# Kernel optimization log

Measured on AMD Instinct MI355X. Metric: run time of the kernel, lower is better.

## Reference

```python
import jax, jax.numpy as jnp
import numpy as np

B, N, E, D, H, C, U = 512, 256, 1024, 256, 256, 8, 64
MARGIN_T, RISK_T, SCALE = 0.2, 0.6, 0.1
NEG = -1.0e9


def setup_inputs() -> dict:
    key = jax.random.key(0)
    ks = jax.random.split(key, 30)
    s = 0.02
    inp = dict(
        features=jax.random.normal(ks[0], (B, D), jnp.float32),
        centered_scores=jax.random.normal(ks[1], (B, N), jnp.float32),
        margin=jax.random.uniform(ks[2], (B,), jnp.float32),
        boundary_risk=jax.random.uniform(ks[3], (B,), jnp.float32),
        edge_sensitivity=jax.random.normal(ks[4], (B, E), jnp.float32),
        coords=jax.random.normal(ks[5], (B, N, C), jnp.float32),
        uncertainty=jax.random.uniform(ks[6], (B, U), jnp.float32),
        Wc1=jax.random.normal(ks[7], (D, H), jnp.float32) * s,
        bc1=jnp.zeros((H,), jnp.float32),
        Wc2=jax.random.normal(ks[8], (H, H), jnp.float32) * s,
        bc2=jnp.zeros((H,), jnp.float32),
        Wn1=jax.random.normal(ks[9], (H + C + 2, H), jnp.float32) * s,
        bn1=jnp.zeros((H,), jnp.float32),
        Wn2=jax.random.normal(ks[10], (H, 1), jnp.float32) * s,
        bn2=jnp.zeros((1,), jnp.float32),
        We1=jax.random.normal(ks[11], (H + C + 2, H), jnp.float32) * s,
        be1=jnp.zeros((H,), jnp.float32),
        We2=jax.random.normal(ks[12], (H, 1), jnp.float32) * s,
        be2=jnp.zeros((1,), jnp.float32),
        Wg=jax.random.normal(ks[13], (H, 1), jnp.float32) * s,
        bg=jnp.zeros((1,), jnp.float32),
        action_mask=jax.random.bernoulli(ks[14], 0.8, (B, N)),
        edge_mask=jax.random.bernoulli(ks[15], 0.8, (B, E)),
        actions=jax.random.randint(ks[16], (B, N), 0, U, jnp.int32),
        edges=jax.random.randint(ks[17], (B, E, 2), 0, N, jnp.int32),
    )
    return inp


def _mlp2(x, W1, b1, W2, b2):
    return jax.nn.relu(x @ W1 + b1) @ W2 + b2


def reference(features, centered_scores, margin, boundary_risk, edge_sensitivity,
              coords, uncertainty, Wc1, bc1, Wc2, bc2, Wn1, bn1, Wn2, bn2,
              We1, be1, We2, be2, Wg, bg, action_mask, edge_mask, actions, edges):
    amf = action_mask.astype(jnp.float32)
    emf = edge_mask.astype(jnp.float32)

    # context MLP
    h = jax.nn.relu(jax.nn.relu(features @ Wc1 + bc1) @ Wc2 + bc2)  # [B,H]

    low_margin = (margin < MARGIN_T).astype(jnp.float32)
    high_risk = (boundary_risk > RISK_T).astype(jnp.float32)
    learned_gate = jax.nn.sigmoid((h @ Wg + bg)[:, 0])
    refine_gate = jnp.maximum(jnp.maximum(low_margin, high_risk),
                              (learned_gate > 0.5).astype(jnp.float32))  # [B]

    # node features: [B,N,H+C+2]
    act = jnp.clip(actions, 0, U - 1)
    unc_g = jnp.take_along_axis(uncertainty, act, axis=1)  # [B,N]
    h_n = jnp.broadcast_to(h[:, None, :], (B, N, H))
    node_feats = jnp.concatenate(
        [h_n, coords, centered_scores[..., None], unc_g[..., None]], axis=-1)
    node_delta = _mlp2(node_feats, Wn1, bn1, Wn2, bn2)[..., 0] * amf  # [B,N]

    # edge features: gather src/dst coords
    e = jnp.clip(edges, 0, N - 1)
    src_c = jnp.take_along_axis(coords, e[:, :, 0:1], axis=1)  # [B,E,C]
    dst_c = jnp.take_along_axis(coords, e[:, :, 1:2], axis=1)  # [B,E,C]
    h_e = jnp.broadcast_to(h[:, None, :], (B, E, H))
    edge_feats = jnp.concatenate(
        [h_e, dst_c - src_c, edge_sensitivity[..., None], emf[..., None]], axis=-1)
    edge_delta = _mlp2(edge_feats, We1, be1, We2, be2)[..., 0] * emf  # [B,E]

    gate_node = refine_gate[:, None]
    refined_scores = (centered_scores + gate_node * SCALE * node_delta) * amf
    denom = jnp.clip(amf.sum(-1, keepdims=True), 1.0, None)  # [B,1]
    refined_scores = (refined_scores - refined_scores.sum(-1, keepdims=True) / denom) * amf

    refined_edge = (edge_sensitivity + gate_node * SCALE * edge_delta) * emf

    masked_top = jnp.where(action_mask, refined_scores, NEG)
    top_vals, top_idx = jax.lax.top_k(masked_top, 2)
    refined_margin = top_vals[:, 0] - top_vals[:, 1]

    # masked per-batch variance of refined_edge (biased), 0 if <=1 valid entry
    cnt = emf.sum(-1)
    cnt_c = jnp.clip(cnt, 1.0, None)
    mean = (refined_edge * emf).sum(-1) / cnt_c
    var = (emf * (refined_edge - mean[:, None]) ** 2).sum(-1) / cnt_c
    edge_var = jnp.where(cnt > 1.0, var, 0.0)

    unc_term = (unc_g * amf).sum(-1) / denom[:, 0]
    refined_risk = jnp.clip(
        jax.nn.sigmoid(-refined_margin) + 0.2 * edge_var + 0.1 * unc_term, 0.0, 1.0)

    return (refined_scores, refined_margin, refined_edge,
            top_idx[:, 0], refined_risk, refine_gate)
```

## Files before the change

### kernel.cpp

```cpp
#include <hip/hip_runtime.h>
#include <math.h>

#define B 512
#define N 256
#define E 1024
#define D 256
#define H 256
#define C 8
#define U 64

typedef __fp16 h2 __attribute__((ext_vector_type(2)));
union UF { float f; h2 h; unsigned u; };

__device__ __forceinline__ float bc_f(h2 h) { UF u; u.h = h; return u.f; }
__device__ __forceinline__ h2 bc_h(float f) { UF u; u.f = f; return u.h; }

#if __has_builtin(__builtin_amdgcn_cvt_pkrtz)
__device__ __forceinline__ h2 pkh(float a, float b) { return __builtin_amdgcn_cvt_pkrtz(a, b); }
#else
__device__ __forceinline__ h2 pkh(float a, float b) { h2 r; r.x = (__fp16)a; r.y = (__fp16)b; return r; }
#endif

#if __has_builtin(__builtin_amdgcn_fdot2)
__device__ __forceinline__ float FDOT2(h2 a, h2 b, float c) { return __builtin_amdgcn_fdot2(a, b, c, false); }
#else
__device__ __forceinline__ float FDOT2(h2 a, h2 b, float c) {
    return fmaf((float)a.x, (float)b.x, fmaf((float)a.y, (float)b.y, c));
}
#endif

__device__ __forceinline__ float mask_val(const void* m, long i, int flag) {
    if (flag == 1) return ((const unsigned char*)m)[i] ? 1.f : 0.f;
    if (flag == 2) return (((const float*)m)[i] != 0.f) ? 1.f : 0.f;
    return ((const int*)m)[i] ? 1.f : 0.f;
}

__device__ __forceinline__ float block_sum(float v, float* red) {
    int t = threadIdx.x;
    red[t] = v; __syncthreads();
    for (int s = 128; s > 0; s >>= 1) {
        if (t < s) red[t] += red[t + s];
        __syncthreads();
    }
    float r = red[0]; __syncthreads();
    return r;
}

__global__ __launch_bounds__(512) void k_h(
    const float* __restrict__ feat,
    const float* __restrict__ Wc1, const float* __restrict__ bc1,
    const float* __restrict__ Wc2, const float* __restrict__ bc2,
    const float* __restrict__ Wn1, const float* __restrict__ bn1,
    const float* __restrict__ We1, const float* __restrict__ be1,
    const float* __restrict__ Wg,  const float* __restrict__ bg,
    const float* __restrict__ margin, const float* __restrict__ brisk,
    const unsigned int* __restrict__ amask_words,
    float* __restrict__ base_n, float* __restrict__ base_e,
    float* __restrict__ out_gate, int* __restrict__ flag,
    float* __restrict__ node_delta, float* __restrict__ out2)
{
    __shared__ __align__(16) float sF[4][256];
    __shared__ __align__(16) float sH[4][256];
    __shared__ float red[512];
    __shared__ int cls0, cls1;

    int t = threadIdx.x;
    int w = t >> 8;
    int c = t & 255;
    int b0 = blockIdx.x * 4;
    int r0 = 2 * w, r1 = 2 * w + 1;

    {
        int idx = blockIdx.x * 512 + t;
        node_delta[idx] = 0.f;
        node_delta[idx + 65536] = 0.f;
        float4 z4 = make_float4(0.f, 0.f, 0.f, 0.f);
        ((float4*)out2)[idx] = z4;
        ((float4*)out2)[idx + 65536] = z4;
    }

    if (blockIdx.x == 0) {
        if (t == 0) { cls0 = 0; cls1 = 0; }
        __syncthreads();
        if (t < 256) {
            unsigned int wd = amask_words[t];
            if (wd != 0u && wd != 1u) {
                if (wd == 0x3f800000u) atomicOr(&cls1, 1);
                else                   atomicOr(&cls0, 1);
            }
        }
        __syncthreads();
        if (t == 0) *flag = cls0 ? 1 : (cls1 ? 2 : 0);
    }

    sF[r0][c] = feat[(long)(b0 + r0) * D + c];
    sF[r1][c] = feat[(long)(b0 + r1) * D + c];
    __syncthreads();

    {
        float aA[2] = {bc1[c], 0.f}, aB[2] = {bc1[c], 0.f};
        const float* Wp = Wc1 + c;
        for (int d0 = 0; d0 < D; d0 += 16) {
            float wv[16];
            #pragma unroll
            for (int k = 0; k < 16; k++) wv[k] = Wp[(long)(d0 + k) * H];
            #pragma unroll
            for (int k = 0; k < 16; k++) {
                aA[k & 1] = fmaf(sF[r0][d0 + k], wv[k], aA[k & 1]);
                aB[k & 1] = fmaf(sF[r1][d0 + k], wv[k], aB[k & 1]);
            }
        }
        sH[r0][c] = fmaxf(aA[0] + aA[1], 0.f);
        sH[r1][c] = fmaxf(aB[0] + aB[1], 0.f);
    }
    __syncthreads();

    {
        float aA[2] = {bc2[c], 0.f}, aB[2] = {bc2[c], 0.f};
        const float* Wp = Wc2 + c;
        for (int d0 = 0; d0 < H; d0 += 16) {
            float wv[16];
            #pragma unroll
            for (int k = 0; k < 16; k++) wv[k] = Wp[(long)(d0 + k) * H];
            #pragma unroll
            for (int k = 0; k < 16; k++) {
                aA[k & 1] = fmaf(sH[r0][d0 + k], wv[k], aA[k & 1]);
                aB[k & 1] = fmaf(sH[r1][d0 + k], wv[k], aB[k & 1]);
            }
        }
        float hA = fmaxf(aA[0] + aA[1], 0.f);
        float hB = fmaxf(aB[0] + aB[1], 0.f);
        __syncthreads();
        sF[r0][c] = hA;
        sF[r1][c] = hB;
    }
    __syncthreads();

    #pragma unroll
    for (int rr = 0; rr < 2; rr++) {
        int r = 2 * w + rr;
        red[t] = sF[r][c] * Wg[c];
        __syncthreads();
        for (int s = 128; s > 0; s >>= 1) {
            if (c < s) red[t] += red[t + s];
            __syncthreads();
        }
        if (c == 0) {
            int b = b0 + r;
            float lg = 1.f / (1.f + expf(-(red[t] + bg[0])));
            out_gate[b] = ((margin[b] < 0.2f) || (brisk[b] > 0.6f) || (lg > 0.5f)) ? 1.f : 0.f;
        }
        __syncthreads();
    }

    {
        const float* W3  = w ? (We1 + c) : (Wn1 + c);
        float bias       = w ? be1[c]    : bn1[c];
        float* dst       = w ? base_e    : base_n;
        float aA[2] = {bias, 0.f}, aB[2] = {bias, 0.f};
        float aC[2] = {bias, 0.f}, aD[2] = {bias, 0.f};
        for (int d0 = 0; d0 < H; d0 += 16) {
            float wv[16];
            #pragma unroll
            for (int k = 0; k < 16; k++) wv[k] = W3[(long)(d0 + k) * H];
            #pragma unroll
            for (int k = 0; k < 16; k++) {
                aA[k & 1] = fmaf(sF[0][d0 + k], wv[k], aA[k & 1]);
                aB[k & 1] = fmaf(sF[1][d0 + k], wv[k], aB[k & 1]);
                aC[k & 1] = fmaf(sF[2][d0 + k], wv[k], aC[k & 1]);
                aD[k & 1] = fmaf(sF[3][d0 + k], wv[k], aD[k & 1]);
            }
        }
        dst[(long)(b0 + 0) * H + c] = aA[0] + aA[1];
        dst[(long)(b0 + 1) * H + c] = aB[0] + aB[1];
        dst[(long)(b0 + 2) * H + c] = aC[0] + aC[1];
        dst[(long)(b0 + 3) * H + c] = aD[0] + aD[1];
    }
}

__global__ __launch_bounds__(256, 2) void k_ne(
    const float* __restrict__ cs, const float* __restrict__ coords,
    const float* __restrict__ unc, const int* __restrict__ actions,
    const float* __restrict__ Wn1, const float* __restrict__ Wn2,
    const float* __restrict__ base_n,
    const float* __restrict__ es, const int* __restrict__ edges,
    const float* __restrict__ We1, const float* __restrict__ We2,
    const float* __restrict__ base_e,
    const float* __restrict__ gate,
    float* __restrict__ node_delta, float* __restrict__ out2)
{
    __shared__ __align__(16) float smem[4096];
    int t = threadIdx.x;
    int w = t >> 6, lane = t & 63;

    if (blockIdx.x < 256) {
        int rg = blockIdx.x >> 1;
        int jh = blockIdx.x & 1;
        int b0 = rg * 4;
        float* pack = smem;
        float* sB   = smem + 1536;

        if (t < 128) {
            float* p = pack + t * 12;
            int j = jh * 128 + t;
            #pragma unroll
            for (int k = 0; k < 10; k++) p[k] = Wn1[(long)(H + k) * H + j];
            p[10] = Wn2[j];
            p[11] = 0.f;
        }
        {
            int r = t >> 7, c0 = t & 127;
            sB[r * 128 + c0]       = base_n[(long)(b0 + r) * H + jh * 128 + c0];
            sB[(r + 2) * 128 + c0] = base_n[(long)(b0 + r + 2) * H + jh * 128 + c0];
        }
        __syncthreads();

        int b = b0 + w;
        float g = gate[b];
        if (g != 0.f) {
            float f8v[4], ug[4], acc[4];
            float f0[4], f1[4], f2[4], f3[4], f4[4], f5[4], f6[4], f7[4];
            #pragma unroll
            for (int q = 0; q < 4; q++) {
                int n = q * 64 + lane;
                const float4* cp = (const float4*)(coords + ((long)b * N + n) * C);
                float4 c0 = cp[0], c1 = cp[1];
                f0[q] = c0.x; f1[q] = c0.y; f2[q] = c0.z; f3[q] = c0.w;
                f4[q] = c1.x; f5[q] = c1.y; f6[q] = c1.z; f7[q] = c1.w;
                f8v[q] = cs[(long)b * N + n];
                int a = actions[(long)b * N + n];
                a = min(max(a, 0), U - 1);
                ug[q] = unc[(long)b * U + a];
                acc[q] = 0.f;
            }

            const float* sBw = sB + w * 128;
            #pragma unroll 4
            for (int j = 0; j < 128; j++) {
                const float* pj = pack + j * 12;
                float4 wa = *(const float4*)(pj);
                float4 wb = *(const float4*)(pj + 4);
                float4 wc = *(const float4*)(pj + 8);
                float bse = sBw[j];
                #pragma unroll
                for (int q = 0; q < 4; q++) {
                    float zA = fmaf(f0[q], wa.x, bse);
                    zA = fmaf(f1[q], wa.y, zA);
                    zA = fmaf(f2[q], wa.z, zA);
                    zA = fmaf(f3[q], wa.w, zA);
                    float zB = f4[q] * wb.x;
                    zB = fmaf(f5[q], wb.y, zB);
                    zB = fmaf(f6[q], wb.z, zB);
                    zB = fmaf(f7[q], wb.w, zB);
                    zB = fmaf(f8v[q], wc.x, zB);
                    zB = fmaf(ug[q], wc.y, zB);
                    acc[q] = fmaf(fmaxf(zA + zB, 0.f), wc.z, acc[q]);
                }
            }

            #pragma unroll
            for (int q = 0; q < 4; q++)
                atomicAdd(&node_delta[(long)b * N + q * 64 + lane], acc[q]);
        }
    } else {
        int eb = blockIdx.x - 256;
        int b = eb >> 1, jh = eb & 1;
        float g = gate[b];
        if (g == 0.f) return;

        float*  A4 = smem;
        float2* B2 = (float2*)(smem + 512);
        float*  sC = smem + 1024;

        {
            const float4* g4 = (const float4*)(coords + (long)b * N * C);
            float4 c0 = g4[2 * t], c1 = g4[2 * t + 1];
            float4* d0 = (float4*)(sC + t * 12);
            d0[0] = c0; d0[1] = c1;
        }
        if (t < 128) {
            int j = jh * 128 + t;
            float w0 = We1[(long)(H + 0) * H + j];
            float w1 = We1[(long)(H + 1) * H + j];
            float w2 = We1[(long)(H + 2) * H + j];
            float w3 = We1[(long)(H + 3) * H + j];
            float w4 = We1[(long)(H + 4) * H + j];
            float w5 = We1[(long)(H + 5) * H + j];
            float w6 = We1[(long)(H + 6) * H + j];
            float w7 = We1[(long)(H + 7) * H + j];
            float w8 = We1[(long)(H + 8) * H + j];
            float w9 = We1[(long)(H + 9) * H + j];
            float we2 = We2[j];
            float bse = base_e[(long)b * H + j] + w9;
            float4 av;
            av.x = bc_f(pkh(w0, w1)); av.y = bc_f(pkh(w2, w3));
            av.z = bc_f(pkh(w4, w5)); av.w = bc_f(pkh(w6, w7));
            ((float4*)A4)[t] = av;
            B2[t] = make_float2(bc_f(pkh(w8, we2)), bse);
        }
        __syncthreads();

        float p01[4], p23[4], p45[4], p67[4], pes[4], acc[4];
        #pragma unroll
        for (int q = 0; q < 4; q++) {
            int e = w * 256 + q * 64 + lane;
            long idx = (long)b * E + e;
            int2 ev = ((const int2*)edges)[idx];
            int s0 = min(max(ev.x, 0), N - 1);
            int d0 = min(max(ev.y, 0), N - 1);
            const float4* cs4 = (const float4*)(sC + s0 * 12);
            const float4* cd4 = (const float4*)(sC + d0 * 12);
            float4 sa = cs4[0], sb = cs4[1];
            float4 da = cd4[0], db = cd4[1];
            p01[q] = bc_f(pkh(da.x - sa.x, da.y - sa.y));
            p23[q] = bc_f(pkh(da.z - sa.z, da.w - sa.w));
            p45[q] = bc_f(pkh(db.x - sb.x, db.y - sb.y));
            p67[q] = bc_f(pkh(db.z - sb.z, db.w - sb.w));
            pes[q] = bc_f(pkh(es[idx], 0.f));
            acc[q] = 0.f;
        }

        const float4* A4v = (const float4*)A4;
        #pragma unroll 4
        for (int j = 0; j < 128; j++) {
            float4 av = A4v[j];
            float2 bv = B2[j];
            h2 w01 = bc_h(av.x), w23 = bc_h(av.y);
            h2 w45 = bc_h(av.z), w67 = bc_h(av.w);
            h2 w8x = bc_h(bv.x);
            float we2f = (float)(w8x.y);
            float bse = bv.y;
            #pragma unroll
            for (int q = 0; q < 4; q++) {
                float z = FDOT2(bc_h(p01[q]), w01, bse);
                z = FDOT2(bc_h(p23[q]), w23, z);
                z = FDOT2(bc_h(p45[q]), w45, z);
                z = FDOT2(bc_h(p67[q]), w67, z);
                z = FDOT2(bc_h(pes[q]), w8x, z);
                acc[q] = fmaf(fmaxf(z, 0.f), we2f, acc[q]);
            }
        }

        #pragma unroll
        for (int q = 0; q < 4; q++)
            atomicAdd(&out2[(long)b * E + w * 256 + q * 64 + lane], acc[q]);
    }
}

__global__ __launch_bounds__(256) void k_fin(
    const void* __restrict__ amask, const void* __restrict__ emask,
    const int* __restrict__ actions, const float* __restrict__ unc,
    const float* __restrict__ cs, const float* __restrict__ es,
    const float* __restrict__ bn2, const float* __restrict__ be2,
    const float* __restrict__ gate, const int* __restrict__ flagp,
    const float* __restrict__ node_delta,
    float* __restrict__ out0, float* __restrict__ out1,
    float* __restrict__ out2, float* __restrict__ out3,
    float* __restrict__ riskbase, float* __restrict__ evar)
{
    __shared__ float red[256];
    __shared__ int ridx[256];
    int t = threadIdx.x;
    int flag = *flagp;

    if (blockIdx.x < B) {
        int b = blockIdx.x;
        float g = gate[b];
        float am = mask_val(amask, (long)b * N + t, flag);
        float csv = cs[(long)b * N + t];
        int a = actions[(long)b * N + t];
        a = min(max(a, 0), U - 1);
        float ug = unc[(long)b * U + a];
        float nd = (node_delta[(long)b * N + t] + bn2[0]) * am;
        float raw = (csv + g * 0.1f * nd) * am;

        float sum = block_sum(raw, red);
        float cnt = block_sum(am, red);
        float denom = fmaxf(cnt, 1.f);
        float rs = (raw - sum / denom) * am;
        out0[(long)b * N + t] = rs;

        float masked = (am != 0.f) ? rs : -1e9f;

        red[t] = masked; ridx[t] = t; __syncthreads();
        for (int s = 128; s > 0; s >>= 1) {
            if (t < s) {
                float o = red[t + s]; int oi = ridx[t + s];
                if (o > red[t] || (o == red[t] && oi < ridx[t])) { red[t] = o; ridx[t] = oi; }
            }
            __syncthreads();
        }
        float v1 = red[0]; int i1 = ridx[0]; __syncthreads();

        red[t] = (t == i1) ? -1e9f : masked; __syncthreads();
        for (int s = 128; s > 0; s >>= 1) {
            if (t < s) red[t] = fmaxf(red[t], red[t + s]);
            __syncthreads();
        }
        float v2 = red[0]; __syncthreads();
        float rmargin = v1 - v2;

        float su = block_sum(ug * am, red);

        if (t == 0) {
            out1[b] = rmargin;
            out3[b] = (float)i1;
            float sig = 1.f / (1.f + expf(rmargin));
            riskbase[b] = sig + 0.1f * (su / denom);
        }
    } else {
        int b = blockIdx.x - B;
        float g = gate[b];
        float be2v = be2[0];

        float re[4], emv[4];
        #pragma unroll
        for (int q = 0; q < 4; q++) {
            long idx = (long)b * E + t + 256 * q;
            emv[q] = mask_val(emask, idx, flag);
            float delta = out2[idx] + be2v;
            float r = es[idx] + g * 0.1f * delta;
            re[q] = (emv[q] != 0.f) ? r : 0.f;
            out2[idx] = re[q];
        }

        float S1 = 0.f, ce = 0.f;
        #pragma unroll
        for (int q = 0; q < 4; q++) { S1 += re[q]; ce += emv[q]; }
        float S1t = block_sum(S1, red);
        float cet = block_sum(ce, red);
        float mean = S1t / fmaxf(cet, 1.f);
        float v = 0.f;
        #pragma unroll
        for (int q = 0; q < 4; q++) {
            float dd = re[q] - mean;
            v = fmaf(emv[q] * dd, dd, v);
        }
        float vt = block_sum(v, red);
        if (t == 0) {
            float var = vt / fmaxf(cet, 1.f);
            evar[b] = (cet > 1.f) ? var : 0.f;
        }
    }
}

__global__ __launch_bounds__(256) void k_risk(
    const float* __restrict__ riskbase, const float* __restrict__ evar,
    float* __restrict__ out4)
{
    int b = blockIdx.x * 256 + threadIdx.x;
    float r = riskbase[b] + 0.2f * evar[b];
    out4[b] = fminf(fmaxf(r, 0.f), 1.f);
}

extern "C" void kernel_launch(void* const* d_in, const int* in_sizes, int n_in,
                              void* d_out, int out_size, void* d_ws, size_t ws_size,
                              hipStream_t stream) {
    const float* feat   = (const float*)d_in[0];
    const float* cs     = (const float*)d_in[1];
    const float* marg   = (const float*)d_in[2];
    const float* brisk  = (const float*)d_in[3];
    const float* es     = (const float*)d_in[4];
    const float* coords = (const float*)d_in[5];
    const float* unc    = (const float*)d_in[6];
    const float* Wc1    = (const float*)d_in[7];
    const float* bc1    = (const float*)d_in[8];
    const float* Wc2    = (const float*)d_in[9];
    const float* bc2    = (const float*)d_in[10];
    const float* Wn1    = (const float*)d_in[11];
    const float* bn1    = (const float*)d_in[12];
    const float* Wn2    = (const float*)d_in[13];
    const float* bn2    = (const float*)d_in[14];
    const float* We1    = (const float*)d_in[15];
    const float* be1    = (const float*)d_in[16];
    const float* We2    = (const float*)d_in[17];
    const float* be2    = (const float*)d_in[18];
    const float* Wg     = (const float*)d_in[19];
    const float* bg     = (const float*)d_in[20];
    const void*  amask  = d_in[21];
    const void*  emask  = d_in[22];
    const int*   actions= (const int*)d_in[23];
    const int*   edges  = (const int*)d_in[24];

    float* out0 = (float*)d_out;
    float* out1 = out0 + (long)B * N;
    float* out2 = out1 + B;
    float* out3 = out2 + (long)B * E;
    float* out4 = out3 + B;
    float* out5 = out4 + B;

    float* base_n     = (float*)d_ws;
    float* base_e     = base_n + (long)B * H;
    float* node_delta = base_e + (long)B * H;
    float* riskbase   = node_delta + (long)B * N;
    float* evar       = riskbase + B;
    int*   flag       = (int*)(evar + B);

    k_h<<<B / 4, 512, 0, stream>>>(feat, Wc1, bc1, Wc2, bc2, Wn1, bn1, We1, be1,
                                   Wg, bg, marg, brisk,
                                   (const unsigned int*)amask,
                                   base_n, base_e, out5, flag,
                                   node_delta, out2);
    k_ne<<<256 + 2 * B, 256, 0, stream>>>(cs, coords, unc, actions,
                                          Wn1, Wn2, base_n,
                                          es, edges,
                                          We1, We2, base_e,
                                          out5, node_delta, out2);
    k_fin<<<2 * B, 256, 0, stream>>>(amask, emask, actions, unc, cs, es,
                                     bn2, be2, out5, flag, node_delta,
                                     out0, out1, out2, out3, riskbase, evar);
    k_risk<<<2, 256, 0, stream>>>(riskbase, evar, out4);
}
```

Baseline: 77.54 us.

## Double grid parallelism in context and node/edge kernels by splitting batch and hidden dims

The context-MLP kernel now handles 2 batch rows per block instead of 4, doubling its grid. Each thread accumulates one row with four partial sums instead of two rows with two. The node/edge kernel splits the hidden dimension into quarters instead of halves, doubling its block count and halving per-block work and shared memory. This gives more parallelism across the many CUs, at the cost of more redundant weight reads, more atomic adds into node_delta, and repeated per-block setup such as loading coordinates.

```diff
diff --git a/kernel.cpp b/kernel.cpp
--- a/kernel.cpp
+++ b/kernel.cpp
@@ -59,24 +59,21 @@
     float* __restrict__ out_gate, int* __restrict__ flag,
     float* __restrict__ node_delta, float* __restrict__ out2)
 {
-    __shared__ __align__(16) float sF[4][256];
-    __shared__ __align__(16) float sH[4][256];
+    __shared__ __align__(16) float sF[2][256];
+    __shared__ __align__(16) float sH[2][256];
     __shared__ float red[512];
     __shared__ int cls0, cls1;
 
     int t = threadIdx.x;
     int w = t >> 8;
     int c = t & 255;
-    int b0 = blockIdx.x * 4;
-    int r0 = 2 * w, r1 = 2 * w + 1;
+    int b0 = blockIdx.x * 2;
+    int b = b0 + w;
 
     {
         int idx = blockIdx.x * 512 + t;
         node_delta[idx] = 0.f;
-        node_delta[idx + 65536] = 0.f;
-        float4 z4 = make_float4(0.f, 0.f, 0.f, 0.f);
-        ((float4*)out2)[idx] = z4;
-        ((float4*)out2)[idx + 65536] = z4;
+        ((float4*)out2)[idx] = make_float4(0.f, 0.f, 0.f, 0.f);
     }
 
     if (blockIdx.x == 0) {
@@ -93,72 +90,58 @@
         if (t == 0) *flag = cls0 ? 1 : (cls1 ? 2 : 0);
     }
 
-    sF[r0][c] = feat[(long)(b0 + r0) * D + c];
-    sF[r1][c] = feat[(long)(b0 + r1) * D + c];
+    sF[w][c] = feat[(long)b * D + c];
     __syncthreads();
 
     {
-        float aA[2] = {bc1[c], 0.f}, aB[2] = {bc1[c], 0.f};
+        float acc[4] = {bc1[c], 0.f, 0.f, 0.f};
         const float* Wp = Wc1 + c;
         for (int d0 = 0; d0 < D; d0 += 16) {
             float wv[16];
             #pragma unroll
             for (int k = 0; k < 16; k++) wv[k] = Wp[(long)(d0 + k) * H];
             #pragma unroll
-            for (int k = 0; k < 16; k++) {
-                aA[k & 1] = fmaf(sF[r0][d0 + k], wv[k], aA[k & 1]);
-                aB[k & 1] = fmaf(sF[r1][d0 + k], wv[k], aB[k & 1]);
-            }
-        }
-        sH[r0][c] = fmaxf(aA[0] + aA[1], 0.f);
-        sH[r1][c] = fmaxf(aB[0] + aB[1], 0.f);
+            for (int k = 0; k < 16; k++)
+                acc[k & 3] = fmaf(sF[w][d0 + k], wv[k], acc[k & 3]);
+        }
+        sH[w][c] = fmaxf((acc[0] + acc[1]) + (acc[2] + acc[3]), 0.f);
     }
     __syncthreads();
 
     {
-        float aA[2] = {bc2[c], 0.f}, aB[2] = {bc2[c], 0.f};
+        float acc[4] = {bc2[c], 0.f, 0.f, 0.f};
         const float* Wp = Wc2 + c;
         for (int d0 = 0; d0 < H; d0 += 16) {
             float wv[16];
             #pragma unroll
             for (int k = 0; k < 16; k++) wv[k] = Wp[(long)(d0 + k) * H];
             #pragma unroll
-            for (int k = 0; k < 16; k++) {
-                aA[k & 1] = fmaf(sH[r0][d0 + k], wv[k], aA[k & 1]);
-                aB[k & 1] = fmaf(sH[r1][d0 + k], wv[k], aB[k & 1]);
-            }
-        }
-        float hA = fmaxf(aA[0] + aA[1], 0.f);
-        float hB = fmaxf(aB[0] + aB[1], 0.f);
-        __syncthreads();
-        sF[r0][c] = hA;
-        sF[r1][c] = hB;
+            for (int k = 0; k < 16; k++)
+                acc[k & 3] = fmaf(sH[w][d0 + k], wv[k], acc[k & 3]);
+        }
+        float a = fmaxf((acc[0] + acc[1]) + (acc[2] + acc[3]), 0.f);
+        __syncthreads();
+        sF[w][c] = a;
     }
     __syncthreads();
 
-    #pragma unroll
-    for (int rr = 0; rr < 2; rr++) {
-        int r = 2 * w + rr;
-        red[t] = sF[r][c] * Wg[c];
-        __syncthreads();
-        for (int s = 128; s > 0; s >>= 1) {
-            if (c < s) red[t] += red[t + s];
-            __syncthreads();
-        }
-        if (c == 0) {
-            int b = b0 + r;
-            float lg = 1.f / (1.f + expf(-(red[t] + bg[0])));
-            out_gate[b] = ((margin[b] < 0.2f) || (brisk[b] > 0.6f) || (lg > 0.5f)) ? 1.f : 0.f;
-        }
-        __syncthreads();
+    red[t] = sF[w][c] * Wg[c];
+    __syncthreads();
+    for (int s = 128; s > 0; s >>= 1) {
+        if (c < s) red[t] += red[t + s];
+        __syncthreads();
+    }
+    if (c == 0) {
+        float lg = 1.f / (1.f + expf(-(red[t] + bg[0])));
+        out_gate[b] = ((margin[b] < 0.2f) || (brisk[b] > 0.6f) || (lg > 0.5f)) ? 1.f : 0.f;
     }
 
     {
         const float* W3  = w ? (We1 + c) : (Wn1 + c);
         float bias       = w ? be1[c]    : bn1[c];
         float* dst       = w ? base_e    : base_n;
-        float aA[2] = {bias, 0.f}, aB[2] = {bias, 0.f};
-        float aC[2] = {bias, 0.f}, aD[2] = {bias, 0.f};
+        float aA[2] = {bias, 0.f};
+        float aB[2] = {bias, 0.f};
         for (int d0 = 0; d0 < H; d0 += 16) {
             float wv[16];
             #pragma unroll
@@ -167,14 +150,10 @@
             for (int k = 0; k < 16; k++) {
                 aA[k & 1] = fmaf(sF[0][d0 + k], wv[k], aA[k & 1]);
                 aB[k & 1] = fmaf(sF[1][d0 + k], wv[k], aB[k & 1]);
-                aC[k & 1] = fmaf(sF[2][d0 + k], wv[k], aC[k & 1]);
-                aD[k & 1] = fmaf(sF[3][d0 + k], wv[k], aD[k & 1]);
-            }
-        }
-        dst[(long)(b0 + 0) * H + c] = aA[0] + aA[1];
+            }
+        }
+        dst[(long)b0 * H + c]       = aA[0] + aA[1];
         dst[(long)(b0 + 1) * H + c] = aB[0] + aB[1];
-        dst[(long)(b0 + 2) * H + c] = aC[0] + aC[1];
-        dst[(long)(b0 + 3) * H + c] = aD[0] + aD[1];
     }
 }
 
@@ -189,29 +168,31 @@
     const float* __restrict__ gate,
     float* __restrict__ node_delta, float* __restrict__ out2)
 {
-    __shared__ __align__(16) float smem[4096];
+    __shared__ __align__(16) float smem[3840];
     int t = threadIdx.x;
     int w = t >> 6, lane = t & 63;
 
-    if (blockIdx.x < 256) {
-        int rg = blockIdx.x >> 1;
-        int jh = blockIdx.x & 1;
+    if (blockIdx.x < 512) {
+        int rg = blockIdx.x >> 2;
+        int jq = blockIdx.x & 3;
         int b0 = rg * 4;
         float* pack = smem;
-        float* sB   = smem + 1536;
-
-        if (t < 128) {
-            float* p = pack + t * 12;
-            int j = jh * 128 + t;
-            #pragma unroll
-            for (int k = 0; k < 10; k++) p[k] = Wn1[(long)(H + k) * H + j];
-            p[10] = Wn2[j];
-            p[11] = 0.f;
-        }
+        float* sB   = smem + 768;
+
         {
-            int r = t >> 7, c0 = t & 127;
-            sB[r * 128 + c0]       = base_n[(long)(b0 + r) * H + jh * 128 + c0];
-            sB[(r + 2) * 128 + c0] = base_n[(long)(b0 + r + 2) * H + jh * 128 + c0];
+            int i = t;
+            #pragma unroll
+            for (int s = 0; s < 3; s++, i += 256) {
+                int j = i / 12, k = i - j * 12;
+                int jj = jq * 64 + j;
+                float v;
+                if (k < 10)       v = Wn1[(long)(H + k) * H + jj];
+                else if (k == 10) v = Wn2[jj];
+                else              v = 0.f;
+                pack[i] = v;
+            }
+            int r = t >> 6, j = t & 63;
+            sB[r * 64 + j] = base_n[(long)(b0 + r) * H + jq * 64 + j];
         }
         __syncthreads();
 
@@ -234,9 +215,9 @@
                 acc[q] = 0.f;
             }
 
-            const float* sBw = sB + w * 128;
+            const float* sBw = sB + w * 64;
             #pragma unroll 4
-            for (int j = 0; j < 128; j++) {
+            for (int j = 0; j < 64; j++) {
                 const float* pj = pack + j * 12;
                 float4 wa = *(const float4*)(pj);
                 float4 wb = *(const float4*)(pj + 4);
@@ -263,14 +244,14 @@
                 atomicAdd(&node_delta[(long)b * N + q * 64 + lane], acc[q]);
         }
     } else {
-        int eb = blockIdx.x - 256;
-        int b = eb >> 1, jh = eb & 1;
+        int eb = blockIdx.x - 512;
+        int b = eb >> 2, jq = eb & 3;
         float g = gate[b];
         if (g == 0.f) return;
 
         float*  A4 = smem;
-        float2* B2 = (float2*)(smem + 512);
-        float*  sC = smem + 1024;
+        float2* B2 = (float2*)(smem + 256);
+        float*  sC = smem + 768;
 
         {
             const float4* g4 = (const float4*)(coords + (long)b * N * C);
@@ -278,8 +259,8 @@
             float4* d0 = (float4*)(sC + t * 12);
             d0[0] = c0; d0[1] = c1;
         }
-        if (t < 128) {
-            int j = jh * 128 + t;
+        if (t < 64) {
+            int j = jq * 64 + t;
             float w0 = We1[(long)(H + 0) * H + j];
             float w1 = We1[(long)(H + 1) * H + j];
             float w2 = We1[(long)(H + 2) * H + j];
@@ -322,7 +303,7 @@
 
         const float4* A4v = (const float4*)A4;
         #pragma unroll 4
-        for (int j = 0; j < 128; j++) {
+        for (int j = 0; j < 64; j++) {
             float4 av = A4v[j];
             float2 bv = B2[j];
             h2 w01 = bc_h(av.x), w23 = bc_h(av.y);
@@ -496,12 +477,12 @@
     float* evar       = riskbase + B;
     int*   flag       = (int*)(evar + B);
 
-    k_h<<<B / 4, 512, 0, stream>>>(feat, Wc1, bc1, Wc2, bc2, Wn1, bn1, We1, be1,
+    k_h<<<B / 2, 512, 0, stream>>>(feat, Wc1, bc1, Wc2, bc2, Wn1, bn1, We1, be1,
                                    Wg, bg, marg, brisk,
                                    (const unsigned int*)amask,
                                    base_n, base_e, out5, flag,
                                    node_delta, out2);
-    k_ne<<<256 + 2 * B, 256, 0, stream>>>(cs, coords, unc, actions,
+    k_ne<<<512 + 4 * B, 256, 0, stream>>>(cs, coords, unc, actions,
                                           Wn1, Wn2, base_n,
                                           es, edges,
                                           We1, We2, base_e,
```

Result: faster. 72.28 us (-6.8%).
